# Kernel optimization log

Measured on AMD Instinct MI355X. Metric: run time of the kernel, lower is better.

The kernel has to match this reference:

```python
import math
import jax, jax.numpy as jnp
import numpy as np

B, S, DIM = 1, 2048, 2880
N_HEADS, N_KV, HD = 64, 8, 64
ROPE_FACTOR = 32.0
THETA = 150000.0
NEG_INF = -1e30


def setup_inputs() -> dict:
    key = jax.random.key(0)
    ks = jax.random.split(key, 12)
    std = 0.02
    x = jax.random.normal(ks[0], (B, S, DIM), jnp.float32)
    # rope cache: (S, 2*HD) = [cos | sin], rotate_half convention (angles duplicated)
    inv_freq = 1.0 / (THETA ** (np.arange(0, HD, 2, dtype=np.float32) / HD))
    angles = np.arange(S, dtype=np.float32)[:, None] * inv_freq[None, :]   # (S, HD/2)
    emb = np.concatenate([angles, angles], axis=-1)                        # (S, HD)
    rope_cache = jnp.asarray(np.concatenate([np.cos(emb), np.sin(emb)], axis=-1))  # (S, 2*HD)
    wq_w = jax.random.normal(ks[1], (N_HEADS * HD, DIM), jnp.float32) * std
    wq_b = jax.random.normal(ks[2], (N_HEADS * HD,), jnp.float32) * std
    wk_w = jax.random.normal(ks[3], (N_KV * HD, DIM), jnp.float32) * std
    wk_b = jax.random.normal(ks[4], (N_KV * HD,), jnp.float32) * std
    wv_w = jax.random.normal(ks[5], (N_KV * HD, DIM), jnp.float32) * std
    wv_b = jax.random.normal(ks[6], (N_KV * HD,), jnp.float32) * std
    wo_w = jax.random.normal(ks[7], (DIM, N_HEADS * HD), jnp.float32) * std
    wo_b = jax.random.normal(ks[8], (DIM,), jnp.float32) * std
    sinks = jax.random.normal(ks[9], (N_HEADS,), jnp.float32) * std
    return {"x": x, "rope_cache": rope_cache, "wq_w": wq_w, "wq_b": wq_b,
            "wk_w": wk_w, "wk_b": wk_b, "wv_w": wv_w, "wv_b": wv_b,
            "wo_w": wo_w, "wo_b": wo_b, "sinks": sinks, "sliding_window": 128}


def _rotate_half(t):
    t1, t2 = t[..., : HD // 2], t[..., HD // 2 :]
    return jnp.concatenate([-t2, t1], axis=-1)


def reference(x, rope_cache, wq_w, wq_b, wk_w, wk_b, wv_w, wv_b, wo_w, wo_b, sinks, sliding_window):
    bsz, seqlen, _ = x.shape
    mscale = 0.1 * math.log(ROPE_FACTOR) + 1.0
    scale = mscale / math.sqrt(HD)

    q = (x @ wq_w.T + wq_b).reshape(bsz, seqlen, N_HEADS, HD)
    k = (x @ wk_w.T + wk_b).reshape(bsz, seqlen, N_KV, HD)
    v = (x @ wv_w.T + wv_b).reshape(bsz, seqlen, N_KV, HD)

    cos = rope_cache[:seqlen, :HD][None, :, None, :]   # (1,S,1,HD)
    sin = rope_cache[:seqlen, HD:][None, :, None, :]
    q = q * cos + _rotate_half(q) * sin
    k = k * cos + _rotate_half(k) * sin

    q = q.transpose(0, 2, 1, 3)                        # (B,H,S,hd)
    n_rep = N_HEADS // N_KV
    k = jnp.repeat(k.transpose(0, 2, 1, 3), n_rep, axis=1)  # GQA expand
    v = jnp.repeat(v.transpose(0, 2, 1, 3), n_rep, axis=1)

    scores = jnp.einsum("bhqd,bhkd->bhqk", q, k) * scale
    i = jnp.arange(seqlen)[:, None]
    j = jnp.arange(seqlen)[None, :]
    mask = (j <= i) & ((i - j) < sliding_window)       # causal + sliding window
    scores = jnp.where(mask[None, None], scores, NEG_INF)

    lse = jax.nn.logsumexp(scores, axis=-1)            # (B,H,S)
    attn = jax.nn.softmax(scores, axis=-1)
    out = jnp.einsum("bhqk,bhkd->bhqd", attn, v)

    sink_scale = jax.nn.sigmoid(lse - sinks[None, :, None])[..., None]
    out = out * sink_scale

    out = out.transpose(0, 2, 1, 3).reshape(bsz, seqlen, N_HEADS * HD)
    return out @ wo_w.T + wo_b
```

## Files before the change

### kernel.cpp

```cpp
#include <hip/hip_runtime.h>
#include <hip/hip_bf16.h>
#include <math.h>
#include <stdint.h>


typedef __bf16 bf16x8 __attribute__((ext_vector_type(8)));
typedef float  f32x4  __attribute__((ext_vector_type(4)));
typedef uint32_t u32x4 __attribute__((ext_vector_type(4)));

#define MFMA_BF16(a,b,c) __builtin_amdgcn_mfma_f32_16x16x32_bf16((a),(b),(c),0,0,0)

#define XB   0L
#define WQB  5898240L
#define WKB  17694720L
#define WVB  19169280L
#define WOB  20643840L
#define QB   32440320L
#define KB   40828928L
#define VB   41877504L

__device__ __forceinline__ void gld_lds16(const void* g, void* l) {
    __builtin_amdgcn_global_load_lds(
        (__attribute__((address_space(1))) void*)(g),
        (__attribute__((address_space(3))) void*)(l), 16, 0, 0);
}

__device__ __forceinline__ bf16x8 ld8f(const float* p) {
    f32x4 a = *(const f32x4*)p;
    f32x4 b = *(const f32x4*)(p + 4);
    bf16x8 r;
#pragma unroll
    for (int t = 0; t < 4; t++) { r[t] = (__bf16)a[t]; r[t + 4] = (__bf16)b[t]; }
    return r;
}

__device__ __forceinline__ uint32_t pack2(float a, float b) {
    __bf16 x = (__bf16)a, y = (__bf16)b;
    return (uint32_t)__builtin_bit_cast(unsigned short, x)
         | ((uint32_t)__builtin_bit_cast(unsigned short, y) << 16);
}

__global__ __launch_bounds__(256) void convert_kernel(
    const float* __restrict__ x,  const float* __restrict__ wq,
    const float* __restrict__ wk, const float* __restrict__ wv,
    const float* __restrict__ wo, __bf16* __restrict__ dst)
{
    long e = ((long)blockIdx.x * 256 + threadIdx.x) * 8;
    const float* src; long off;
    if      (e <  WQB) { src = x;  off = e; }
    else if (e <  WKB) { src = wq; off = e - WQB; }
    else if (e <  WVB) { src = wk; off = e - WKB; }
    else if (e <  WOB) { src = wv; off = e - WVB; }
    else               { src = wo; off = e - WOB; }
    *(bf16x8*)(dst + e) = ld8f(src + off);
}

__device__ __forceinline__ void stage256(
    const __bf16* pa0, const __bf16* pb0, const __bf16* pb1,
    const __bf16* pb2, const __bf16* pb3, size_t aStep, int kk,
    __bf16* Asb, __bf16* Bsb, int tid)
{
    gld_lds16(pa0 + kk,             Asb + (tid        ) * 8);
    gld_lds16(pa0 + aStep + kk,     Asb + (tid +  512 ) * 8);
    gld_lds16(pa0 + 2 * aStep + kk, Asb + (tid + 1024 ) * 8);
    gld_lds16(pa0 + 3 * aStep + kk, Asb + (tid + 1536 ) * 8);
    gld_lds16(pb0 + kk,             Bsb + (tid        ) * 8);
    gld_lds16(pb1 + kk,             Bsb + (tid +  512 ) * 8);
    gld_lds16(pb2 + kk,             Bsb + (tid + 1024 ) * 8);
    gld_lds16(pb3 + kk,             Bsb + (tid + 1536 ) * 8);
}

__device__ __forceinline__ void gemm256(
    const __bf16* __restrict__ A, const __bf16* __restrict__ W,
    const float* __restrict__ bias, __bf16* __restrict__ C,
    int N, int Ks, int kBeg, int kEnd, int m0, int n0,
    __bf16* As, __bf16* Bs)
{
    const int tid  = threadIdx.x;
    const int lane = tid & 63;
    const int wv   = tid >> 6;
    const int wr   = wv >> 2;
    const int wc   = wv & 3;
    const int quad = lane >> 4;
    const int c    = lane & 15;

    const int srow = tid >> 3;
    const int scg2 = (tid & 7) ^ (srow & 7);

    const __bf16* pa0 = A + (size_t)(m0 + srow) * Ks + scg2 * 8;
    const size_t aStep = (size_t)64 * Ks;
    const __bf16* pb[4];
#pragma unroll
    for (int i = 0; i < 4; i++) {
        int br = n0 + srow + 64 * i; if (br > N - 1) br = N - 1;
        pb[i] = W + (size_t)br * Ks + scg2 * 8;
    }

    const int NT = (kEnd - kBeg) >> 6;

    f32x4 acc[8][4];
#pragma unroll
    for (int i = 0; i < 8; i++)
#pragma unroll
        for (int j = 0; j < 4; j++) acc[i][j] = (f32x4){0.f, 0.f, 0.f, 0.f};

    stage256(pa0, pb[0], pb[1], pb[2], pb[3], aStep, kBeg,      As,         Bs,         tid);
    stage256(pa0, pb[0], pb[1], pb[2], pb[3], aStep, kBeg + 64, As + 16384, Bs + 16384, tid);
    asm volatile("s_waitcnt vmcnt(8)" ::: "memory");
    __builtin_amdgcn_sched_barrier(0);
    __builtin_amdgcn_s_barrier();

    const int fxor = c & 7;

    for (int t = 0; t < NT; ++t) {
        __builtin_amdgcn_sched_barrier(0);
        const __bf16* Ab = As + (t & 1) * 16384;
        const __bf16* Bb = Bs + (t & 1) * 16384;
#pragma unroll
        for (int kt = 0; kt < 2; kt++) {
            const int ko = ((kt * 4 + quad) ^ fxor) * 8;
            bf16x8 af[8], bfv[4];
#pragma unroll
            for (int i = 0; i < 8; i++)
                af[i] = *(const bf16x8*)&Ab[(wr * 128 + i * 16 + c) * 64 + ko];
#pragma unroll
            for (int j = 0; j < 4; j++)
                bfv[j] = *(const bf16x8*)&Bb[(wc * 64 + j * 16 + c) * 64 + ko];
            __builtin_amdgcn_s_setprio(1);
#pragma unroll
            for (int i = 0; i < 8; i++)
#pragma unroll
                for (int j = 0; j < 4; j++)
                    acc[i][j] = MFMA_BF16(af[i], bfv[j], acc[i][j]);
            __builtin_amdgcn_s_setprio(0);
        }
        __builtin_amdgcn_sched_barrier(0);
        __builtin_amdgcn_s_barrier();
        if (t + 2 < NT) {
            stage256(pa0, pb[0], pb[1], pb[2], pb[3], aStep, kBeg + (t + 2) * 64,
                     As + (t & 1) * 16384, Bs + (t & 1) * 16384, tid);
            asm volatile("s_waitcnt vmcnt(8)" ::: "memory");
        } else {
            asm volatile("s_waitcnt vmcnt(0)" ::: "memory");
        }
        __builtin_amdgcn_sched_barrier(0);
        __builtin_amdgcn_s_barrier();
    }

#pragma unroll
    for (int j = 0; j < 4; j++) {
        int col = n0 + wc * 64 + j * 16 + c;
        if (col >= N) continue;
        float bv = bias ? bias[col] : 0.0f;
#pragma unroll
        for (int i = 0; i < 8; i++) {
            int row = m0 + wr * 128 + i * 16 + quad * 4;
#pragma unroll
            for (int r = 0; r < 4; r++)
                C[(size_t)(row + r) * N + col] = (__bf16)(acc[i][j][r] + bv);
        }
    }
}

__global__ __launch_bounds__(512, 2) void qkv_kernel(
    const __bf16* __restrict__ x,
    const __bf16* __restrict__ wq, const float* __restrict__ bq,
    const __bf16* __restrict__ wk, const float* __restrict__ bk,
    const __bf16* __restrict__ wv, const float* __restrict__ bv,
    __bf16* __restrict__ qo, __bf16* __restrict__ ko, __bf16* __restrict__ vo)
{
    __shared__ __align__(16) __bf16 As[2 * 16384], Bs[2 * 16384];
    const int lin = blockIdx.y * 8 + blockIdx.x;
    const int wg  = (lin & 7) * 20 + (lin >> 3);
    const int m0  = (wg & 7) * 256;
    const int by2 = wg >> 3;
    const __bf16 *W; const float* bias; __bf16* C; int N, n0;
    if (by2 < 16)      { W = wq; bias = bq; C = qo; N = 4096; n0 = by2 * 256; }
    else if (by2 < 18) { W = wk; bias = bk; C = ko; N = 512;  n0 = (by2 - 16) * 256; }
    else               { W = wv; bias = bv; C = vo; N = 512;  n0 = (by2 - 18) * 256; }
    gemm256(x, W, bias, C, N, 2880, 0, 2880, m0, n0, As, Bs);
}

__global__ __launch_bounds__(512, 2) void oproj_kernel(
    const __bf16* __restrict__ a, const __bf16* __restrict__ w,
    __bf16* __restrict__ p0, __bf16* __restrict__ p1)
{
    __shared__ __align__(16) __bf16 As[2 * 16384], Bs[2 * 16384];
    const int z = blockIdx.z;
    __bf16* C = z ? p1 : p0;
    const int lin = blockIdx.y * 8 + blockIdx.x;
    const int wg  = (lin & 7) * 12 + (lin >> 3);
    const int m0  = (wg & 7) * 256;
    const int by2 = wg >> 3;
    gemm256(a, w, nullptr, C, 2880, 4096, z * 2048, (z + 1) * 2048,
            m0, by2 * 256, As, Bs);
}

__global__ __launch_bounds__(256) void reduce_kernel(
    const __bf16* __restrict__ p0, const __bf16* __restrict__ p1,
    const float* __restrict__ bo, float* __restrict__ out)
{
    long e = ((long)blockIdx.x * 256 + threadIdx.x) * 8;
    int col = (int)(e % 2880L);
    bf16x8 a = *(const bf16x8*)(p0 + e);
    bf16x8 b = *(const bf16x8*)(p1 + e);
    f32x4 o0, o1;
#pragma unroll
    for (int t = 0; t < 4; t++) {
        o0[t] = (float)a[t]     + (float)b[t]     + bo[col + t];
        o1[t] = (float)a[4 + t] + (float)b[4 + t] + bo[col + 4 + t];
    }
    *(f32x4*)(out + e)     = o0;
    *(f32x4*)(out + e + 4) = o1;
}

template<int F>
__device__ __forceinline__ void attn_f_step(
    const __bf16* __restrict__ Ks, const __bf16* __restrict__ Vt,
    __bf16* __restrict__ q, bf16x8 qf0, bf16x8 qf1,
    int i0, int h, int k0, float sk,
    int c, int quad, int laneA, int laneB, bool hiSel, int db)
{
    f32x4 acc9[9];
#pragma unroll
    for (int jj = 0; jj < 9; jj++) acc9[jj] = (f32x4){0.f, 0.f, 0.f, 0.f};
    __builtin_amdgcn_s_setprio(1);
#pragma unroll
    for (int jj = 0; jj < 9; jj++) {
        const int j = F + jj;
        bf16x8 kf0 = *(const bf16x8*)&Ks[(j * 16 + c) * 72 + quad * 8];
        bf16x8 kf1 = *(const bf16x8*)&Ks[(j * 16 + c) * 72 + 32 + quad * 8];
        acc9[jj] = MFMA_BF16(kf0, qf0, acc9[jj]);
        acc9[jj] = MFMA_BF16(kf1, qf1, acc9[jj]);
    }
    __builtin_amdgcn_s_setprio(0);

    const int jgb = k0 + F * 16 + quad * 4;
    float rmax = -3.0e4f;
#pragma unroll
    for (int jj = 0; jj < 9; jj++)
#pragma unroll
        for (int r = 0; r < 4; r++) {
            int d  = db  - jj * 16 - r;
            int jg = jgb + jj * 16 + r;
            bool ok = ((unsigned)d < 128u) && (jg >= 0);
            float vv = ok ? acc9[jj][r] : -3.0e4f;
            acc9[jj][r] = vv;
            rmax = fmaxf(rmax, vv);
        }
    rmax = fmaxf(rmax, __shfl_xor(rmax, 16));
    rmax = fmaxf(rmax, __shfl_xor(rmax, 32));

    float rs = 0.f;
#pragma unroll
    for (int jj = 0; jj < 9; jj++)
#pragma unroll
        for (int r = 0; r < 4; r++) {
            float e = __expf(acc9[jj][r] - rmax);
            acc9[jj][r] = e;
            rs += e;
        }
    rs += __shfl_xor(rs, 16);
    rs += __shfl_xor(rs, 32);

    float s   = fmaxf(rs, 1e-20f);
    float lse = rmax + __logf(s);
    float fac = 1.f / ((1.f + __expf(sk - lse)) * s);

    uint32_t pk[20];
#pragma unroll
    for (int t = 0; t < 20; t++) pk[t] = 0;
#pragma unroll
    for (int jj = 0; jj < 9; jj++) {
        const int li = (F & 1) ? (2 * jj + 2) : (2 * jj);
        pk[li]     = pack2(acc9[jj][0] * fac, acc9[jj][1] * fac);
        pk[li + 1] = pack2(acc9[jj][2] * fac, acc9[jj][3] * fac);
    }

    f32x4 acc2[4];
#pragma unroll
    for (int jd = 0; jd < 4; jd++) acc2[jd] = (f32x4){0.f, 0.f, 0.f, 0.f};
#pragma unroll
    for (int kk = 0; kk < 5; kk++) {
        const int kt = (F >> 1) + kk;
        uint32_t l0  = (uint32_t)__shfl((int)pk[4 * kk],     laneA);
        uint32_t h0  = (uint32_t)__shfl((int)pk[4 * kk + 1], laneA);
        uint32_t l0b = (uint32_t)__shfl((int)pk[4 * kk],     laneB);
        uint32_t h0b = (uint32_t)__shfl((int)pk[4 * kk + 1], laneB);
        uint32_t l1  = (uint32_t)__shfl((int)pk[4 * kk + 2], laneA);
        uint32_t h1  = (uint32_t)__shfl((int)pk[4 * kk + 3], laneA);
        uint32_t l1b = (uint32_t)__shfl((int)pk[4 * kk + 2], laneB);
        uint32_t h1b = (uint32_t)__shfl((int)pk[4 * kk + 3], laneB);
        u32x4 wvv = { hiSel ? l1  : l0,  hiSel ? h1  : h0,
                      hiSel ? l1b : l0b, hiSel ? h1b : h0b };
        bf16x8 pa = __builtin_bit_cast(bf16x8, wvv);
        __builtin_amdgcn_s_setprio(1);
#pragma unroll
        for (int jd = 0; jd < 4; jd++) {
            bf16x8 bv = *(const bf16x8*)&Vt[(jd * 16 + c) * 200 + kt * 32 + quad * 8];
            acc2[jd] = MFMA_BF16(pa, bv, acc2[jd]);
        }
        __builtin_amdgcn_s_setprio(0);
    }

#pragma unroll
    for (int jd = 0; jd < 4; jd++)
#pragma unroll
        for (int r = 0; r < 4; r++)
            q[(size_t)(i0 + F * 16 + quad * 4 + r) * 4096 + h * 64 + jd * 16 + c]
                = (__bf16)acc2[jd][r];
}

__global__ __launch_bounds__(512) void attn_kernel(
    __bf16* __restrict__ q, const __bf16* __restrict__ k,
    const __bf16* __restrict__ v, const float* __restrict__ sinks,
    const float* __restrict__ rope)
{
    __shared__ __align__(16) __bf16 Ks[192 * 72];
    __shared__ __align__(16) __bf16 Vt[64 * 200];

    const int tid = threadIdx.x, lane = tid & 63, w = tid >> 6;
    const int quad = lane >> 4, c = lane & 15;
    const int i0  = blockIdx.x * 64;
    const int kvh = blockIdx.y;
    const int h   = kvh * 8 + w;
    const int k0  = i0 - 128;
    const float scale = 0.16832169878499658f;

#pragma unroll
    for (int it = 0; it < 2; it++) {
        int unit = it * 512 + tid;
        if (unit < 768) {
            int krow = unit >> 2;
            int kdg  = (unit & 3) * 8;
            int j = k0 + krow; if (j < 0) j = 0;
            const __bf16* gp = k + (size_t)j * 512 + kvh * 64 + kdg;
            bf16x8 x1 = *(const bf16x8*)(gp);
            bf16x8 x2 = *(const bf16x8*)(gp + 32);
            const float* rc = rope + (size_t)j * 128 + kdg;
            bf16x8 o1, o2;
#pragma unroll
            for (int t = 0; t < 8; t++) {
                float cc = rc[t], si = rc[64 + t];
                float a = (float)x1[t], b = (float)x2[t];
                o1[t] = (__bf16)(a * cc - b * si);
                o2[t] = (__bf16)(b * cc + a * si);
            }
            *(bf16x8*)&Ks[krow * 72 + kdg]      = o1;
            *(bf16x8*)&Ks[krow * 72 + kdg + 32] = o2;
        }
    }

    {
        const int vrow = tid & 63;
        const int d0   = (tid >> 6) * 8;
#pragma unroll
        for (int it = 0; it < 3; it++) {
            int s = it * 64 + vrow;
            int j = k0 + s; if (j < 0) j = 0;
            bf16x8 t = *(const bf16x8*)(v + (size_t)j * 512 + kvh * 64 + d0);
#pragma unroll
            for (int u = 0; u < 8; u++) Vt[(d0 + u) * 200 + s] = t[u];
        }
    }

    bf16x8 qf[4][2];
#pragma unroll
    for (int f = 0; f < 4; f++) {
        const int row = i0 + f * 16 + c;
        const __bf16* gp = q + (size_t)row * 4096 + h * 64 + quad * 8;
        bf16x8 x1 = *(const bf16x8*)(gp);
        bf16x8 x2 = *(const bf16x8*)(gp + 32);
        const float* rc = rope + (size_t)row * 128 + quad * 8;
        bf16x8 o1, o2;
#pragma unroll
        for (int t = 0; t < 8; t++) {
            float cc = rc[t] * scale, si = rc[64 + t] * scale;
            float a = (float)x1[t], b = (float)x2[t];
            o1[t] = (__bf16)(a * cc - b * si);
            o2[t] = (__bf16)(b * cc + a * si);
        }
        qf[f][0] = o1; qf[f][1] = o2;
    }

    __syncthreads();

    const float sk   = sinks[h];
    const int laneA  = ((quad & 1) << 5) + c;
    const int laneB  = laneA + 16;
    const bool hiSel = (quad >> 1) != 0;
    const int db     = 128 + c - quad * 4;

    attn_f_step<0>(Ks, Vt, q, qf[0][0], qf[0][1], i0, h, k0, sk, c, quad, laneA, laneB, hiSel, db);
    attn_f_step<1>(Ks, Vt, q, qf[1][0], qf[1][1], i0, h, k0, sk, c, quad, laneA, laneB, hiSel, db);
    attn_f_step<2>(Ks, Vt, q, qf[2][0], qf[2][1], i0, h, k0, sk, c, quad, laneA, laneB, hiSel, db);
    attn_f_step<3>(Ks, Vt, q, qf[3][0], qf[3][1], i0, h, k0, sk, c, quad, laneA, laneB, hiSel, db);
}

extern "C" void kernel_launch(void* const* d_in, const int* in_sizes, int n_in,
                              void* d_out, int out_size, void* d_ws, size_t ws_size,
                              hipStream_t stream) {
    const float* x    = (const float*)d_in[0];
    const float* rope = (const float*)d_in[1];
    const float* wq   = (const float*)d_in[2];
    const float* bq   = (const float*)d_in[3];
    const float* wk   = (const float*)d_in[4];
    const float* bk   = (const float*)d_in[5];
    const float* wv   = (const float*)d_in[6];
    const float* bv   = (const float*)d_in[7];
    const float* wo   = (const float*)d_in[8];
    const float* bo   = (const float*)d_in[9];
    const float* sk   = (const float*)d_in[10];
    float* out = (float*)d_out;

    __bf16* wsb = (__bf16*)d_ws;
    __bf16* xb  = wsb + XB;
    __bf16* wqb = wsb + WQB;
    __bf16* wkb = wsb + WKB;
    __bf16* wvb = wsb + WVB;
    __bf16* wob = wsb + WOB;
    __bf16* qb  = wsb + QB;
    __bf16* kb  = wsb + KB;
    __bf16* vb  = wsb + VB;
    __bf16* po0 = wsb + 0L;
    __bf16* po1 = wsb + 5898240L;

    convert_kernel<<<15840, 256, 0, stream>>>(x, wq, wk, wv, wo, xb);
    qkv_kernel<<<dim3(8, 20), 512, 0, stream>>>(xb, wqb, bq, wkb, bk, wvb, bv,
                                                qb, kb, vb);
    attn_kernel<<<dim3(32, 8), 512, 0, stream>>>(qb, kb, vb, sk, rope);
    oproj_kernel<<<dim3(8, 12, 2), 512, 0, stream>>>(qb, wob, po0, po1);
    reduce_kernel<<<2880, 256, 0, stream>>>(po0, po1, bo, out);
}
```

Before: 363.2 us.

## Split GEMM main loop into four quadrant phases with interleaved half-tile prefetch

Restructures the 256x256 bf16 GEMM main loop into four sub-phases, each computing one quadrant of the warp's accumulator tile. Global-to-LDS loads are split into half-tiles that are issued between phases, so memory traffic interleaves with MFMA work at a finer grain. The LDS layout changes so that each warp row or column group reads its own 8192-element half, and register fragments are reduced to 4x2 per phase. This adds more barriers per iteration and more intricate buffer-reuse ordering, which risks extra synchronisation stalls or hazards.

```diff
diff --git a/kernel.cpp b/kernel.cpp
--- a/kernel.cpp
+++ b/kernel.cpp
@@ -55,19 +55,11 @@
     *(bf16x8*)(dst + e) = ld8f(src + off);
 }
 
-__device__ __forceinline__ void stage256(
-    const __bf16* pa0, const __bf16* pb0, const __bf16* pb1,
-    const __bf16* pb2, const __bf16* pb3, size_t aStep, int kk,
-    __bf16* Asb, __bf16* Bsb, int tid)
-{
-    gld_lds16(pa0 + kk,             Asb + (tid        ) * 8);
-    gld_lds16(pa0 + aStep + kk,     Asb + (tid +  512 ) * 8);
-    gld_lds16(pa0 + 2 * aStep + kk, Asb + (tid + 1024 ) * 8);
-    gld_lds16(pa0 + 3 * aStep + kk, Asb + (tid + 1536 ) * 8);
-    gld_lds16(pb0 + kk,             Bsb + (tid        ) * 8);
-    gld_lds16(pb1 + kk,             Bsb + (tid +  512 ) * 8);
-    gld_lds16(pb2 + kk,             Bsb + (tid + 1024 ) * 8);
-    gld_lds16(pb3 + kk,             Bsb + (tid + 1536 ) * 8);
+__device__ __forceinline__ void stage_half(
+    const __bf16* p0, const __bf16* p1, int kk, __bf16* dst, int tid)
+{
+    gld_lds16(p0 + kk, dst + tid * 8);
+    gld_lds16(p1 + kk, dst + 4096 + tid * 8);
 }
 
 __device__ __forceinline__ void gemm256(
@@ -83,17 +75,18 @@
     const int wc   = wv & 3;
     const int quad = lane >> 4;
     const int c    = lane & 15;
+    const int fxor = c & 7;
+    const int lrB  = (wc & 1) * 64;
 
     const int srow = tid >> 3;
-    const int scg2 = (tid & 7) ^ (srow & 7);
-
-    const __bf16* pa0 = A + (size_t)(m0 + srow) * Ks + scg2 * 8;
-    const size_t aStep = (size_t)64 * Ks;
-    const __bf16* pb[4];
-#pragma unroll
-    for (int i = 0; i < 4; i++) {
-        int br = n0 + srow + 64 * i; if (br > N - 1) br = N - 1;
-        pb[i] = W + (size_t)br * Ks + scg2 * 8;
+    const int scg  = (tid & 7) ^ (srow & 7);
+
+    const __bf16* pa[4]; const __bf16* pb[4];
+#pragma unroll
+    for (int g = 0; g < 4; g++) {
+        pa[g] = A + (size_t)(m0 + g * 64 + srow) * Ks + scg * 8;
+        int br = n0 + g * 64 + srow; if (br > N - 1) br = N - 1;
+        pb[g] = W + (size_t)br * Ks + scg * 8;
     }
 
     const int NT = (kEnd - kBeg) >> 6;
@@ -104,45 +97,126 @@
 #pragma unroll
         for (int j = 0; j < 4; j++) acc[i][j] = (f32x4){0.f, 0.f, 0.f, 0.f};
 
-    stage256(pa0, pb[0], pb[1], pb[2], pb[3], aStep, kBeg,      As,         Bs,         tid);
-    stage256(pa0, pb[0], pb[1], pb[2], pb[3], aStep, kBeg + 64, As + 16384, Bs + 16384, tid);
-    asm volatile("s_waitcnt vmcnt(8)" ::: "memory");
+    stage_half(pb[0], pb[1], kBeg, Bs,        tid);
+    stage_half(pa[0], pa[1], kBeg, As,        tid);
+    stage_half(pa[2], pa[3], kBeg, As + 8192, tid);
+    stage_half(pb[2], pb[3], kBeg, Bs + 8192, tid);
+    if (NT > 1) {
+        stage_half(pb[0], pb[1], kBeg + 64, Bs + 16384, tid);
+        stage_half(pa[0], pa[1], kBeg + 64, As + 16384, tid);
+        asm volatile("s_waitcnt vmcnt(4)" ::: "memory");
+    } else {
+        asm volatile("s_waitcnt vmcnt(0)" ::: "memory");
+    }
     __builtin_amdgcn_sched_barrier(0);
     __builtin_amdgcn_s_barrier();
 
-    const int fxor = c & 7;
+    bf16x8 af[4][2], bb[4][2];
 
     for (int t = 0; t < NT; ++t) {
-        __builtin_amdgcn_sched_barrier(0);
-        const __bf16* Ab = As + (t & 1) * 16384;
-        const __bf16* Bb = Bs + (t & 1) * 16384;
-#pragma unroll
-        for (int kt = 0; kt < 2; kt++) {
-            const int ko = ((kt * 4 + quad) ^ fxor) * 8;
-            bf16x8 af[8], bfv[4];
-#pragma unroll
-            for (int i = 0; i < 8; i++)
-                af[i] = *(const bf16x8*)&Ab[(wr * 128 + i * 16 + c) * 64 + ko];
-#pragma unroll
-            for (int j = 0; j < 4; j++)
-                bfv[j] = *(const bf16x8*)&Bb[(wc * 64 + j * 16 + c) * 64 + ko];
-            __builtin_amdgcn_s_setprio(1);
-#pragma unroll
-            for (int i = 0; i < 8; i++)
-#pragma unroll
-                for (int j = 0; j < 4; j++)
-                    acc[i][j] = MFMA_BF16(af[i], bfv[j], acc[i][j]);
-            __builtin_amdgcn_s_setprio(0);
-        }
-        __builtin_amdgcn_sched_barrier(0);
-        __builtin_amdgcn_s_barrier();
+        const int d = t & 1;
+        const __bf16* Ab = As + d * 16384 + wr * 8192;
+        const __bf16* Bb = Bs + d * 16384 + (wc >> 1) * 8192;
+        __bf16* Asn = As + (d ^ 1) * 16384;
+        __bf16* Bsn = Bs + (d ^ 1) * 16384;
+        __bf16* Asc = As + d * 16384;
+        __bf16* Bsc = Bs + d * 16384;
+        const int kk1 = kBeg + (t + 1) * 64;
+        const int kk2 = kBeg + (t + 2) * 64;
+
+        __builtin_amdgcn_sched_barrier(0);
+#pragma unroll
+        for (int m = 0; m < 4; m++)
+#pragma unroll
+            for (int kt = 0; kt < 2; kt++)
+                af[m][kt] = *(const bf16x8*)&Ab[(m * 16 + c) * 64 + (((kt * 4 + quad) ^ fxor) * 8)];
+#pragma unroll
+        for (int j = 0; j < 2; j++)
+#pragma unroll
+            for (int kt = 0; kt < 2; kt++)
+                bb[j][kt] = *(const bf16x8*)&Bb[(lrB + j * 16 + c) * 64 + (((kt * 4 + quad) ^ fxor) * 8)];
+        if (t + 1 < NT) stage_half(pa[2], pa[3], kk1, Asn + 8192, tid);
+        __builtin_amdgcn_sched_barrier(0);
+        __builtin_amdgcn_s_barrier();
+        asm volatile("s_waitcnt lgkmcnt(0)" ::: "memory");
+        __builtin_amdgcn_sched_barrier(0);
+        __builtin_amdgcn_s_setprio(1);
+#pragma unroll
+        for (int i = 0; i < 4; i++)
+#pragma unroll
+            for (int j = 0; j < 2; j++)
+#pragma unroll
+                for (int kt = 0; kt < 2; kt++)
+                    acc[i][j] = MFMA_BF16(af[i][kt], bb[j][kt], acc[i][j]);
+        __builtin_amdgcn_s_setprio(0);
+        __builtin_amdgcn_sched_barrier(0);
+        __builtin_amdgcn_s_barrier();
+
+        __builtin_amdgcn_sched_barrier(0);
+#pragma unroll
+        for (int j = 2; j < 4; j++)
+#pragma unroll
+            for (int kt = 0; kt < 2; kt++)
+                bb[j][kt] = *(const bf16x8*)&Bb[(lrB + j * 16 + c) * 64 + (((kt * 4 + quad) ^ fxor) * 8)];
+        if (t + 1 < NT) stage_half(pb[2], pb[3], kk1, Bsn + 8192, tid);
+        __builtin_amdgcn_sched_barrier(0);
+        __builtin_amdgcn_s_barrier();
+        asm volatile("s_waitcnt lgkmcnt(0)" ::: "memory");
+        __builtin_amdgcn_sched_barrier(0);
+        __builtin_amdgcn_s_setprio(1);
+#pragma unroll
+        for (int i = 0; i < 4; i++)
+#pragma unroll
+            for (int j = 2; j < 4; j++)
+#pragma unroll
+                for (int kt = 0; kt < 2; kt++)
+                    acc[i][j] = MFMA_BF16(af[i][kt], bb[j][kt], acc[i][j]);
+        __builtin_amdgcn_s_setprio(0);
+        __builtin_amdgcn_sched_barrier(0);
+        __builtin_amdgcn_s_barrier();
+
+        __builtin_amdgcn_sched_barrier(0);
+#pragma unroll
+        for (int m = 0; m < 4; m++)
+#pragma unroll
+            for (int kt = 0; kt < 2; kt++)
+                af[m][kt] = *(const bf16x8*)&Ab[((m + 4) * 16 + c) * 64 + (((kt * 4 + quad) ^ fxor) * 8)];
+        if (t + 2 < NT) stage_half(pb[0], pb[1], kk2, Bsc, tid);
+        __builtin_amdgcn_sched_barrier(0);
+        __builtin_amdgcn_s_barrier();
+        asm volatile("s_waitcnt lgkmcnt(0)" ::: "memory");
+        __builtin_amdgcn_sched_barrier(0);
+        __builtin_amdgcn_s_setprio(1);
+#pragma unroll
+        for (int i = 0; i < 4; i++)
+#pragma unroll
+            for (int j = 0; j < 2; j++)
+#pragma unroll
+                for (int kt = 0; kt < 2; kt++)
+                    acc[i + 4][j] = MFMA_BF16(af[i][kt], bb[j][kt], acc[i + 4][j]);
+        __builtin_amdgcn_s_setprio(0);
+        __builtin_amdgcn_sched_barrier(0);
+        __builtin_amdgcn_s_barrier();
+
+        __builtin_amdgcn_sched_barrier(0);
         if (t + 2 < NT) {
-            stage256(pa0, pb[0], pb[1], pb[2], pb[3], aStep, kBeg + (t + 2) * 64,
-                     As + (t & 1) * 16384, Bs + (t & 1) * 16384, tid);
-            asm volatile("s_waitcnt vmcnt(8)" ::: "memory");
-        } else {
+            stage_half(pa[0], pa[1], kk2, Asc, tid);
+            asm volatile("s_waitcnt vmcnt(4)" ::: "memory");
+        } else if (t + 1 < NT) {
             asm volatile("s_waitcnt vmcnt(0)" ::: "memory");
         }
+        __builtin_amdgcn_sched_barrier(0);
+        __builtin_amdgcn_s_barrier();
+        __builtin_amdgcn_sched_barrier(0);
+        __builtin_amdgcn_s_setprio(1);
+#pragma unroll
+        for (int i = 0; i < 4; i++)
+#pragma unroll
+            for (int j = 2; j < 4; j++)
+#pragma unroll
+                for (int kt = 0; kt < 2; kt++)
+                    acc[i + 4][j] = MFMA_BF16(af[i][kt], bb[j][kt], acc[i + 4][j]);
+        __builtin_amdgcn_s_setprio(0);
         __builtin_amdgcn_sched_barrier(0);
         __builtin_amdgcn_s_barrier();
     }
```

Result: no change. 361.3 us (-0.5%).
